# Kernel tuning notes

Measured on AMD Instinct MI355X. Metric: run time of the kernel, lower is better.

The kernel has to match this reference:

```python
import jax, jax.numpy as jnp
import numpy as np


def setup_inputs() -> dict:
    key = jax.random.key(0)
    k1, _ = jax.random.split(key)
    x = jax.random.normal(k1, (8, 128, 56, 56), dtype=jnp.float32)
    gamma = jnp.array(0.5, dtype=jnp.float32)  # learned scalar (init gamma=0.5)
    return {"x": x, "gamma": gamma}


def reference(x, gamma):
    # conv=False path: query/key/value convs are Identity, so Q=K=V=x flattened.
    B, C, H, W = x.shape
    N = H * W
    v = x.reshape(B, C, N)                          # [B, C, N]
    # energy[b, i, j] = sum_c x[b, c, i] * x[b, c, j]  (Q^T K)
    energy = jnp.einsum('bci,bcj->bij', v, v)       # [B, N, N]
    # multiplicative mask: zero out the diagonal BEFORE softmax (not -inf)
    mask = 1.0 - jnp.eye(N, dtype=energy.dtype)
    attention = jax.nn.softmax(energy * mask, axis=-1)  # [B, N, N]
    # out = bmm(V, attention): out[b, c, j] = sum_i v[b, c, i] * attention[b, i, j]
    out = jnp.einsum('bci,bij->bcj', v, attention)  # [B, C, N]
    out = jax.nn.relu(out).reshape(B, C, H, W)
    y = gamma * out + x
    return (y, out, x, gamma)
```

## Files before the change

### kernel.cpp

```cpp
#include <hip/hip_runtime.h>
#include <math.h>

#define Bb 8
#define Cc 128
#define Nn 3136
#define Np 3200
#define Mm (Bb*Cc*Nn)
#define PADX 136
#define PADV 72
#define SHIFT 44.0f

typedef unsigned short u16;
typedef unsigned int   u32;
typedef __attribute__((ext_vector_type(8)))  u16      u16x8;
typedef __attribute__((ext_vector_type(8)))  _Float16 f16x8;
typedef __attribute__((ext_vector_type(4)))  _Float16 f16x4;
typedef __attribute__((ext_vector_type(4)))  float    f32x4;
typedef __attribute__((ext_vector_type(16))) float    f32x16;

__global__ __launch_bounds__(256) void prep_kernel(const float* __restrict__ x,
                                                   const float* __restrict__ gamma_p,
                                                   float* __restrict__ out,
                                                   u16* __restrict__ xt,
                                                   u16* __restrict__ xc,
                                                   float* __restrict__ row_d) {
    const int bx = blockIdx.x;
    const int b = bx / 50, nblk = bx % 50;
    const int t = threadIdx.x;

    if (nblk == 49) {
        const u16x8 z8 = {0, 0, 0, 0, 0, 0, 0, 0};
        #pragma unroll
        for (int it = 0; it < 4; ++it) {
            const int idx = it * 256 + t, row = idx / 17, seg = idx % 17;
            *(u16x8*)&xt[(size_t)(b * Np + Nn + row) * PADX + seg * 8] = z8;
        }
        if (t < 64) {
            const int idx = 1024 + t, row = idx / 17, seg = idx % 17;
            *(u16x8*)&xt[(size_t)(b * Np + Nn + row) * PADX + seg * 8] = z8;
        }
        #pragma unroll
        for (int it = 0; it < 4; ++it) {
            const int idx = it * 256 + t, c = idx >> 3, seg = idx & 7;
            *(u16x8*)&xc[(size_t)(b * Cc + c) * Np + Nn + seg * 8] = z8;
        }
        if (t < 64) row_d[b * Np + Nn + t] = 1.0f;
        return;
    }

    __shared__ float lx[Cc][65];
    const int n0 = nblk * 64;

    #pragma unroll 8
    for (int r = 0; r < 32; ++r) {
        const int c = r * 4 + (t >> 6);
        const int g = (b * Cc + c) * Nn + n0 + (t & 63);
        const float v = x[g];
        lx[c][t & 63] = v;
        out[(size_t)2 * Mm + g] = v;
    }
    __syncthreads();

    {
        const int nl = t & 63, cseg = t >> 6;
        u16x8 hv[4];
        #pragma unroll
        for (int cc = 0; cc < 32; ++cc) {
            const _Float16 hh = (_Float16)lx[cseg * 32 + cc][nl];
            hv[cc >> 3][cc & 7] = __builtin_bit_cast(u16, hh);
        }
        const size_t base = (size_t)(b * Np + n0 + nl) * PADX + cseg * 32;
        #pragma unroll
        for (int k = 0; k < 4; ++k) *(u16x8*)&xt[base + k * 8] = hv[k];
    }
    {
        const int c = t >> 1, half = t & 1;
        u16x8 hv[4];
        #pragma unroll
        for (int k = 0; k < 32; ++k) {
            const _Float16 hh = (_Float16)lx[c][half * 32 + k];
            hv[k >> 3][k & 7] = __builtin_bit_cast(u16, hh);
        }
        const size_t base = (size_t)(b * Cc + c) * Np + n0 + half * 32;
        #pragma unroll
        for (int k = 0; k < 4; ++k) *(u16x8*)&xc[base + k * 8] = hv[k];
    }
    if (bx == 0 && t == 0) out[(size_t)3 * Mm] = gamma_p[0];
}

__global__ __launch_bounds__(256, 3) void stats_kernel(const u16* __restrict__ xt,
                                                       float* __restrict__ row_d) {
    __shared__ u16 s_jt[64 * PADX];

    const int bx = blockIdx.x;
    const int b = bx / 98, rem = bx % 98;
    const int i0 = (rem >> 1) * 64, jh = rem & 1;
    const int t = threadIdx.x;
    const int w = t >> 6, l = t & 63, lane = l & 31, h = l >> 5;
    const int igrp = w & 1, jsub = w >> 1;

    f16x8 Bf[8];
    {
        const size_t rb = (size_t)(b * Np + i0 + igrp * 32 + lane) * PADX + h * 8;
        #pragma unroll
        for (int kk = 0; kk < 8; ++kk)
            Bf[kk] = *(const f16x8*)&xt[rb + kk * 16];
    }

    float sa = 0.0f, sb = 0.0f;
    const int jt0 = jh * 25;

    for (int jt = jt0; jt < jt0 + 25; ++jt) {
        const int j0 = jt * 64;
        __syncthreads();
        {
            const u16* src = xt + (size_t)(b * Np + j0) * PADX;
            u16x8 tv[4], tv4;
            #pragma unroll
            for (int it = 0; it < 4; ++it)
                tv[it] = *(const u16x8*)&src[(it * 256 + t) * 8];
            if (t < 64) tv4 = *(const u16x8*)&src[(1024 + t) * 8];
            #pragma unroll
            for (int it = 0; it < 4; ++it)
                *(u16x8*)&s_jt[(it * 256 + t) * 8] = tv[it];
            if (t < 64) *(u16x8*)&s_jt[(1024 + t) * 8] = tv4;
        }
        __syncthreads();

        f32x16 ea, eb;
        #pragma unroll
        for (int r = 0; r < 16; ++r) { ea[r] = 0.0f; eb[r] = 0.0f; }
        const int arow = (jsub * 32 + lane) * PADX + h * 8;
        #pragma unroll
        for (int kk = 0; kk < 4; ++kk) {
            const f16x8 A0 = *(const f16x8*)&s_jt[arow + (2 * kk) * 16];
            const f16x8 A1 = *(const f16x8*)&s_jt[arow + (2 * kk + 1) * 16];
            ea = __builtin_amdgcn_mfma_f32_32x32x16_f16(A0, Bf[2 * kk], ea, 0, 0, 0);
            eb = __builtin_amdgcn_mfma_f32_32x32x16_f16(A1, Bf[2 * kk + 1], eb, 0, 0, 0);
        }

        const bool diag = (j0 == i0) && (jsub == igrp);
        #pragma unroll
        for (int r = 0; r < 16; ++r) {
            const int mrow = (r & 3) + 8 * (r >> 2) + 4 * h;
            float v = ea[r] + eb[r];
            if (diag && (mrow == lane)) v = 0.0f;
            if (r & 1) sb += __expf(v - SHIFT); else sa += __expf(v - SHIFT);
        }
    }

    float ssum = sa + sb;
    ssum += __shfl_xor(ssum, 32, 64);
    if (h == 0) atomicAdd(&row_d[b * Np + i0 + igrp * 32 + lane], ssum);
}

__global__ __launch_bounds__(256, 3) void out_kernel(const float* __restrict__ x,
                                                     const u16* __restrict__ xt,
                                                     const u16* __restrict__ xc,
                                                     const float* __restrict__ row_d,
                                                     const float* __restrict__ gamma_p,
                                                     float* __restrict__ out) {
    __shared__ u16 s_xt[64 * PADX];
    __shared__ u16 s_xc[Cc * PADV];
    __shared__ u16 s_pt[64 * PADV];

    const int bx = blockIdx.x;
    const int b = bx / 49, j0 = (bx % 49) * 64;
    const int t = threadIdx.x;
    const int w = t >> 6, l = t & 63, lane = l & 31, h = l >> 5;
    const int isub = w & 1, jgrp = w >> 1;
    const int jg = w & 1,  cp = w >> 1;
    const u16* __restrict__ xtb = xt + (size_t)b * Np * PADX;
    const u16* __restrict__ xcb = xc + (size_t)b * Cc * Np;

    f16x8 Bj[8];
    {
        const size_t rb = (size_t)(j0 + jgrp * 32 + lane) * PADX + h * 8;
        #pragma unroll
        for (int kk = 0; kk < 8; ++kk)
            Bj[kk] = *(const f16x8*)&xtb[rb + kk * 16];
    }

    f32x16 oa, ob;
    #pragma unroll
    for (int r = 0; r < 16; ++r) { oa[r] = 0.0f; ob[r] = 0.0f; }

    for (int ti = 0; ti < 50; ++ti) {
        const int i0g = ti * 64;
        __syncthreads();
        {
            const u16* srct = xtb + (size_t)i0g * PADX;
            u16x8 vt[4], vt4, vcr[4];
            #pragma unroll
            for (int it = 0; it < 4; ++it) {
                vt[it] = *(const u16x8*)&srct[(it * 256 + t) * 8];
                const int q = it * 256 + t;
                vcr[it] = *(const u16x8*)&xcb[(size_t)(q >> 3) * Np + i0g + (q & 7) * 8];
            }
            if (t < 64) vt4 = *(const u16x8*)&srct[(1024 + t) * 8];
            #pragma unroll
            for (int it = 0; it < 4; ++it) {
                *(u16x8*)&s_xt[(it * 256 + t) * 8] = vt[it];
                const int q = it * 256 + t;
                *(u16x8*)&s_xc[(q >> 3) * PADV + (q & 7) * 8] = vcr[it];
            }
            if (t < 64) *(u16x8*)&s_xt[(1024 + t) * 8] = vt4;
        }
        __syncthreads();

        f32x16 ea, eb;
        #pragma unroll
        for (int r = 0; r < 16; ++r) { ea[r] = 0.0f; eb[r] = 0.0f; }
        const int arow = (isub * 32 + lane) * PADX + h * 8;
        #pragma unroll
        for (int kk = 0; kk < 4; ++kk) {
            const f16x8 A0 = *(const f16x8*)&s_xt[arow + (2 * kk) * 16];
            const f16x8 A1 = *(const f16x8*)&s_xt[arow + (2 * kk + 1) * 16];
            ea = __builtin_amdgcn_mfma_f32_32x32x16_f16(A0, Bj[2 * kk], ea, 0, 0, 0);
            eb = __builtin_amdgcn_mfma_f32_32x32x16_f16(A1, Bj[2 * kk + 1], eb, 0, 0, 0);
        }

        const bool mayDiag = (j0 < i0g + 64) && (i0g < j0 + 64);
        const int ptbase = (jgrp * 32 + lane) * PADV + isub * 32;
        #pragma unroll
        for (int q = 0; q < 4; ++q) {
            const f32x4 dq = *(const f32x4*)&row_d[b * Np + i0g + isub * 32 + q * 8 + h * 4];
            f16x4 pv;
            #pragma unroll
            for (int r = 0; r < 4; ++r) {
                const int m = q * 8 + h * 4 + r;
                float v = ea[q * 4 + r] + eb[q * 4 + r];
                if (mayDiag && (i0g + isub * 32 + m == j0 + jgrp * 32 + lane)) v = 0.0f;
                pv[r] = (_Float16)(__expf(v - SHIFT) * __builtin_amdgcn_rcpf(dq[r]));
            }
            *(f16x4*)&s_pt[ptbase + q * 8 + h * 4] = pv;
        }
        __syncthreads();

        const int pbrow = (jg * 32 + lane) * PADV + h * 8;
        const int va0 = (cp * 64 + lane) * PADV + h * 8;
        const int va1 = va0 + 32 * PADV;
        #pragma unroll
        for (int kk = 0; kk < 4; ++kk) {
            const f16x8 Bp  = *(const f16x8*)&s_pt[pbrow + kk * 16];
            const f16x8 Av0 = *(const f16x8*)&s_xc[va0 + kk * 16];
            const f16x8 Av1 = *(const f16x8*)&s_xc[va1 + kk * 16];
            oa = __builtin_amdgcn_mfma_f32_32x32x16_f16(Av0, Bp, oa, 0, 0, 0);
            ob = __builtin_amdgcn_mfma_f32_32x32x16_f16(Av1, Bp, ob, 0, 0, 0);
        }
    }

    const float gamma = gamma_p[0];
    #pragma unroll
    for (int r = 0; r < 16; ++r) {
        const int mrow = (r & 3) + 8 * (r >> 2) + 4 * h;
        const int jj = j0 + jg * 32 + lane;
        {
            const int c = cp * 64 + mrow;
            const size_t pos = (size_t)(b * Cc + c) * Nn + jj;
            const float o = fmaxf(oa[r], 0.0f);
            out[pos] = fmaf(gamma, o, x[pos]);
            out[(size_t)Mm + pos] = o;
        }
        {
            const int c = cp * 64 + 32 + mrow;
            const size_t pos = (size_t)(b * Cc + c) * Nn + jj;
            const float o = fmaxf(ob[r], 0.0f);
            out[pos] = fmaf(gamma, o, x[pos]);
            out[(size_t)Mm + pos] = o;
        }
    }
}

extern "C" void kernel_launch(void* const* d_in, const int* in_sizes, int n_in,
                              void* d_out, int out_size, void* d_ws, size_t ws_size,
                              hipStream_t stream) {
    const float* x       = (const float*)d_in[0];
    const float* gamma_p = (const float*)d_in[1];
    float* out = (float*)d_out;

    float* row_d = (float*)d_ws;
    u16* xt = (u16*)((char*)d_ws + (1 << 17));
    u16* xc = xt + (size_t)Bb * Np * PADX;

    hipMemsetAsync(row_d, 0, (size_t)Bb * Np * sizeof(float), stream);
    prep_kernel <<<400, 256, 0, stream>>>(x, gamma_p, out, xt, xc, row_d);
    stats_kernel<<<784, 256, 0, stream>>>(xt, row_d);
    out_kernel  <<<392, 256, 0, stream>>>(x, xt, xc, row_d, gamma_p, out);
}
```

Before: 205.3 us.

## Split attention reductions across more blocks and add a finishing epilogue kernel

```diff
diff --git a/kernel.cpp b/kernel.cpp
--- a/kernel.cpp
+++ b/kernel.cpp
@@ -93,8 +93,8 @@
     __shared__ u16 s_jt[64 * PADX];
 
     const int bx = blockIdx.x;
-    const int b = bx / 98, rem = bx % 98;
-    const int i0 = (rem >> 1) * 64, jh = rem & 1;
+    const int b = bx / 196, rem = bx % 196;
+    const int i0 = (rem >> 2) * 64, jq = rem & 3;
     const int t = threadIdx.x;
     const int w = t >> 6, l = t & 63, lane = l & 31, h = l >> 5;
     const int igrp = w & 1, jsub = w >> 1;
@@ -108,9 +108,10 @@
     }
 
     float sa = 0.0f, sb = 0.0f;
-    const int jt0 = jh * 25;
-
-    for (int jt = jt0; jt < jt0 + 25; ++jt) {
+    const int jt0 = jq * 12 + (jq < 2 ? jq : 2);
+    const int jcnt = 12 + (jq < 2 ? 1 : 0);
+
+    for (int jt = jt0; jt < jt0 + jcnt; ++jt) {
         const int j0 = jt * 64;
         __syncthreads();
         {
@@ -154,18 +155,17 @@
     if (h == 0) atomicAdd(&row_d[b * Np + i0 + igrp * 32 + lane], ssum);
 }
 
-__global__ __launch_bounds__(256, 3) void out_kernel(const float* __restrict__ x,
-                                                     const u16* __restrict__ xt,
+__global__ __launch_bounds__(256, 3) void out_kernel(const u16* __restrict__ xt,
                                                      const u16* __restrict__ xc,
                                                      const float* __restrict__ row_d,
-                                                     const float* __restrict__ gamma_p,
                                                      float* __restrict__ out) {
     __shared__ u16 s_xt[64 * PADX];
     __shared__ u16 s_xc[Cc * PADV];
     __shared__ u16 s_pt[64 * PADV];
 
     const int bx = blockIdx.x;
-    const int b = bx / 49, j0 = (bx % 49) * 64;
+    const int b = bx / 98, rem = bx % 98;
+    const int j0 = (rem >> 1) * 64, ih = rem & 1;
     const int t = threadIdx.x;
     const int w = t >> 6, l = t & 63, lane = l & 31, h = l >> 5;
     const int isub = w & 1, jgrp = w >> 1;
@@ -185,7 +185,7 @@
     #pragma unroll
     for (int r = 0; r < 16; ++r) { oa[r] = 0.0f; ob[r] = 0.0f; }
 
-    for (int ti = 0; ti < 50; ++ti) {
+    for (int ti = ih * 25; ti < ih * 25 + 25; ++ti) {
         const int i0g = ti * 64;
         __syncthreads();
         {
@@ -250,7 +250,6 @@
         }
     }
 
-    const float gamma = gamma_p[0];
     #pragma unroll
     for (int r = 0; r < 16; ++r) {
         const int mrow = (r & 3) + 8 * (r >> 2) + 4 * h;
@@ -258,18 +257,33 @@
         {
             const int c = cp * 64 + mrow;
             const size_t pos = (size_t)(b * Cc + c) * Nn + jj;
-            const float o = fmaxf(oa[r], 0.0f);
-            out[pos] = fmaf(gamma, o, x[pos]);
-            out[(size_t)Mm + pos] = o;
+            out[(size_t)ih * Mm + pos] = oa[r];
         }
         {
             const int c = cp * 64 + 32 + mrow;
             const size_t pos = (size_t)(b * Cc + c) * Nn + jj;
-            const float o = fmaxf(ob[r], 0.0f);
-            out[pos] = fmaf(gamma, o, x[pos]);
-            out[(size_t)Mm + pos] = o;
-        }
-    }
+            out[(size_t)ih * Mm + pos] = ob[r];
+        }
+    }
+}
+
+__global__ __launch_bounds__(256) void finish_kernel(const float* __restrict__ x,
+                                                     const float* __restrict__ gamma_p,
+                                                     float* __restrict__ out) {
+    const float gamma = gamma_p[0];
+    const size_t base = ((size_t)blockIdx.x * 256 + threadIdx.x) * 4;
+    const f32x4 pa = *(const f32x4*)&out[base];
+    const f32x4 pb = *(const f32x4*)&out[(size_t)Mm + base];
+    const f32x4 xv = *(const f32x4*)&x[base];
+    f32x4 yo, oo;
+    #pragma unroll
+    for (int r = 0; r < 4; ++r) {
+        const float o = fmaxf(pa[r] + pb[r], 0.0f);
+        oo[r] = o;
+        yo[r] = fmaf(gamma, o, xv[r]);
+    }
+    *(f32x4*)&out[base] = yo;
+    *(f32x4*)&out[(size_t)Mm + base] = oo;
 }
 
 extern "C" void kernel_launch(void* const* d_in, const int* in_sizes, int n_in,
@@ -284,7 +298,8 @@
     u16* xc = xt + (size_t)Bb * Np * PADX;
 
     hipMemsetAsync(row_d, 0, (size_t)Bb * Np * sizeof(float), stream);
-    prep_kernel <<<400, 256, 0, stream>>>(x, gamma_p, out, xt, xc, row_d);
-    stats_kernel<<<784, 256, 0, stream>>>(xt, row_d);
-    out_kernel  <<<392, 256, 0, stream>>>(x, xt, xc, row_d, gamma_p, out);
-}
+    prep_kernel  <<<400, 256, 0, stream>>>(x, gamma_p, out, xt, xc, row_d);
+    stats_kernel <<<1568, 256, 0, stream>>>(xt, row_d);
+    out_kernel   <<<784, 256, 0, stream>>>(xt, xc, row_d, out);
+    finish_kernel<<<3136, 256, 0, stream>>>(x, gamma_p, out);
+}
```

Result: slower. 215.2 us (+4.8%).
